# Optimization experiments

Measured on AMD Instinct MI355X. Metric: run time of the kernel, lower is better.

## Reference

```python
import jax, jax.numpy as jnp
import numpy as np

B, N = 8, 8192
S_ATTN, S_NONE = 128, 384          # npoint = (npoint_all=512, npoint_none_attn=384) -> npoint_attn=128
S = S_ATTN + S_NONE
NSAMPLE = 64
RADIUS = 0.4
D_FEAT = 64
MLP = [64, 64, 128]
IN_CH = 3 + D_FEAT


def fps(pts, K):
    # pytorch3d.sample_farthest_points, start index 0, full lengths. pts: [B,N,3]
    B_, N_, _ = pts.shape
    def body(carry, _):
        min_d2, last = carry
        lp = jnp.take_along_axis(pts, last[:, None, None], axis=1)      # [B,1,3]
        d2 = jnp.sum((pts - lp) ** 2, -1)                               # [B,N]
        min_d2 = jnp.minimum(min_d2, d2)
        nxt = jnp.argmax(min_d2, -1).astype(jnp.int32)
        return (min_d2, nxt), last
    init = (jnp.full((B_, N_), jnp.float32(1e10)), jnp.zeros((B_,), jnp.int32))
    _, idxs = jax.lax.scan(body, init, None, length=K)
    idxs = idxs.T                                                       # [B,K]
    sampled = jnp.take_along_axis(pts, idxs[..., None], axis=1)         # [B,K,3]
    return sampled, idxs


def ball_query(query, pts, K, radius):
    # pytorch3d.ball_query: first K points with d2 < r^2 in index order; idx pad=-1, nn pad=0.
    d2 = jnp.sum((query[:, :, None, :] - pts[:, None, :, :]) ** 2, -1)  # [B,S,N]
    mask = d2 < radius * radius
    order = jnp.cumsum(mask.astype(jnp.int32), -1) - 1
    slot = jnp.where(mask & (order < K), order, K)                      # overflow -> dump slot K
    n_ids = jnp.broadcast_to(jnp.arange(pts.shape[1], dtype=jnp.int32), slot.shape)
    def scatter_row(slot_row, ids_row):
        return jnp.full((K + 1,), -1, jnp.int32).at[slot_row].set(ids_row)[:K]
    idx = jax.vmap(jax.vmap(scatter_row))(slot, n_ids)                  # [B,S,K]
    valid = idx >= 0
    gathered = jax.vmap(lambda p, i: p[i])(pts, jnp.where(valid, idx, 0))  # [B,S,K,3]
    nn = jnp.where(valid[..., None], gathered, 0.0)
    return idx, nn


def _forward(xyz, points, attention, ws, bs):
    xyz_t = xyz.transpose(0, 2, 1)            # [B,N,3]
    pts_t = points.transpose(0, 2, 1)         # [B,N,D]
    attn_t = attention.transpose(0, 2, 1)     # [B,N,1]

    attn_xyz = attn_t * xyz_t
    none_xyz = (1.0 - attn_t) * xyz_t
    new_attn_xyz, idx_a = fps(attn_xyz, S_ATTN)
    new_none_xyz, idx_n = fps(none_xyz, S_NONE)
    new_xyz = jnp.concatenate([new_attn_xyz, new_none_xyz], axis=1)     # [B,S,3]
    fps_idx = jnp.concatenate([idx_a, idx_n], axis=1)                   # [B,S]
    new_attention = jnp.take_along_axis(attn_t, fps_idx[..., None], axis=1)  # [B,S,1]

    idx, grouped_xyz = ball_query(new_xyz, xyz_t, NSAMPLE, RADIUS)
    grouped_norm = grouped_xyz - new_xyz[:, :, None, :]                 # [B,S,K,3]
    gather_idx = jnp.where(idx < 0, N - 1, idx)   # torch index -1 wraps to last point
    grouped_pts = jax.vmap(lambda p, i: p[i])(pts_t, gather_idx)        # [B,S,K,D]
    feat = jnp.concatenate([grouped_norm, grouped_pts], -1)             # [B,S,K,3+D]

    x = feat.transpose(0, 3, 2, 1)                                      # [B,C,K,S]
    for w, b in zip(ws, bs):                                            # 1x1 Conv2d + ReLU
        x = jax.nn.relu(jnp.einsum('oc,bcks->boks', w, x) + b[None, :, None, None])
    new_points = jnp.max(x, axis=2)                                     # MaxPool over nsample -> [B,C',S]
    return new_xyz.transpose(0, 2, 1), new_points, new_attention.transpose(0, 2, 1)


def setup_inputs() -> dict:
    key = jax.random.key(0)
    ks = jax.random.split(key, 8)
    xyz = jax.random.normal(ks[0], (B, 3, N), jnp.float32)
    points = jax.random.normal(ks[1], (B, D_FEAT, N), jnp.float32)
    attention = jnp.round(jax.random.uniform(ks[2], (B, 1, N), jnp.float32))  # 0/1 mask
    inp = {'xyz': xyz, 'points': points, 'attention': attention}
    last = IN_CH
    for i, oc in enumerate(MLP):
        inp[f'w{i}'] = jax.random.normal(ks[3 + i], (oc, last), jnp.float32) / np.float32(np.sqrt(last))
        inp[f'b{i}'] = jnp.zeros((oc,), jnp.float32)
        last = oc
    return inp


def reference(xyz, points, attention, w0, b0, w1, b1, w2, b2):
    return _forward(xyz, points, attention, (w0, w1, w2), (b0, b1, b2))
```

## Files before the change

kernel.cpp:

```cpp
#include <hip/hip_runtime.h>
#include <cstdint>
#include <cstddef>

#define NB 8
#define NPTS 8192
#define S_TOT 512
#define NSAMP 64
#define DFEAT 64
#define INCH 67
#define SLOTS 17
#define CCAP (SLOTS * 256)
#define TDONE 1060
#define BALLW 13568

typedef __attribute__((ext_vector_type(8))) short v8s;
typedef __attribute__((ext_vector_type(4))) short v4s;
typedef __attribute__((ext_vector_type(4))) float v4f;

__device__ __forceinline__ float d2_exact(float ax, float ay, float az,
                                          float bx, float by, float bz) {
    float dx = __fsub_rn(ax, bx);
    float dy = __fsub_rn(ay, by);
    float dz = __fsub_rn(az, bz);
    return __fadd_rn(__fadd_rn(__fmul_rn(dx, dx), __fmul_rn(dy, dy)), __fmul_rn(dz, dz));
}

__device__ __forceinline__ unsigned short f2b(float f) {
    unsigned u = __float_as_uint(f);
    return (unsigned short)((u + 0x7fffu + ((u >> 16) & 1u)) >> 16);
}

__device__ __forceinline__ void st_wt_f32(float* p, float v) {
    __hip_atomic_store(p, v, __ATOMIC_RELAXED, __HIP_MEMORY_SCOPE_AGENT);
}
__device__ __forceinline__ void st_wt_u32(unsigned* p, unsigned v) {
    __hip_atomic_store(p, v, __ATOMIC_RELAXED, __HIP_MEMORY_SCOPE_AGENT);
}

template <int CTRL>
__device__ __forceinline__ unsigned long long dpp_max_u64(unsigned long long k) {
    int lo = (int)(unsigned)(k & 0xffffffffull);
    int hi = (int)(unsigned)(k >> 32);
    int slo = __builtin_amdgcn_update_dpp(lo, lo, CTRL, 0xf, 0xf, false);
    int shi = __builtin_amdgcn_update_dpp(hi, hi, CTRL, 0xf, 0xf, false);
    unsigned long long o = ((unsigned long long)(unsigned)shi << 32) | (unsigned)slo;
    return (o > k) ? o : k;
}

__device__ __forceinline__ void ball_one(
    const float* __restrict__ xyz,
    const unsigned short* __restrict__ ptsTh,
    const unsigned short* __restrict__ wp,
    const float* __restrict__ b0, const float* __restrict__ b1,
    const float* __restrict__ b2,
    const float* __restrict__ out0, float* __restrict__ out1,
    int b, int sg, int lane, short* sBuf, int* s_idx)
{
    const float R2 = (float)(0.4 * 0.4);
    int col = lane & 15, quad = lane >> 4, kq = quad * 8;

    const float* xb = xyz + (size_t)b * 3 * NPTS;
    float qx = out0[(size_t)b * 3 * S_TOT + sg];
    float qy = out0[(size_t)b * 3 * S_TOT + S_TOT + sg];
    float qz = out0[(size_t)b * 3 * S_TOT + 2 * S_TOT + sg];

    unsigned long long* s_mask = (unsigned long long*)sBuf;

#pragma unroll 8
    for (int j = 0; j < 128; j++) {
        int n = j * 64 + lane;
        float d2 = d2_exact(qx, qy, qz, xb[n], xb[NPTS + n], xb[2 * NPTS + n]);
        unsigned long long m = __ballot(d2 < R2);
        if (lane == 0) s_mask[j] = m;
    }

    unsigned long long m0 = s_mask[lane];
    unsigned long long m1 = s_mask[64 + lane];
    int c0 = (int)__popcll(m0), c1 = (int)__popcll(m1);
    int i0 = c0;
#pragma unroll
    for (int off = 1; off <= 32; off <<= 1) {
        int t = __shfl_up(i0, off);
        if (lane >= off) i0 += t;
    }
    int T0 = __shfl(i0, 63);
    int i1 = c1;
#pragma unroll
    for (int off = 1; off <= 32; off <<= 1) {
        int t = __shfl_up(i1, off);
        if (lane >= off) i1 += t;
    }
    int total = T0 + __shfl(i1, 63);
    int p0 = i0 - c0;
    int p1 = T0 + i1 - c1;

    {
        int base = p0, org = lane * 64;
        while (m0 && base < NSAMP) {
            int bp = __ffsll((long long)m0) - 1;
            s_idx[base++] = org + bp;
            m0 &= m0 - 1;
        }
        base = p1; org = (64 + lane) * 64;
        while (m1 && base < NSAMP) {
            int bp = __ffsll((long long)m1) - 1;
            s_idx[base++] = org + bp;
            m1 &= m1 - 1;
        }
    }
    int cnt = (total > NSAMP) ? NSAMP : total;

    int nb = (lane < cnt) ? s_idx[lane] : -1;
    float nx_ = 0.f, ny_ = 0.f, nz_ = 0.f;
    if (nb >= 0) { nx_ = xb[nb]; ny_ = xb[NPTS + nb]; nz_ = xb[2 * NPTS + nb]; }
    float fx = nx_ - qx, fy = ny_ - qy, fz = nz_ - qz;
    int row = (nb < 0) ? (NPTS - 1) : nb;

    {
        const unsigned short* ph = ptsTh + ((size_t)b * NPTS + row) * DFEAT;
        short* xr = &sBuf[lane * 104];
#pragma unroll
        for (int i = 0; i < 8; i++)
            *(v8s*)(xr + i * 8) = *(const v8s*)(ph + i * 8);
#pragma unroll
        for (int i = 0; i < 5; i++)
            *(v8s*)(xr + 64 + i * 8) = (v8s)0;
        v4s xyzp;
        xyzp[0] = (short)f2b(fx); xyzp[1] = (short)f2b(fy);
        xyzp[2] = (short)f2b(fz); xyzp[3] = 0;
        *(v4s*)(xr + 64) = xyzp;
    }

    const v8s* wpv = (const v8s*)wp;

    v4f acc[4][4];
#pragma unroll
    for (int nt = 0; nt < 4; nt++) {
        float bb = b0[nt * 16 + col];
#pragma unroll
        for (int mt = 0; mt < 4; mt++) acc[mt][nt] = (v4f){bb, bb, bb, bb};
    }
#pragma unroll
    for (int kt = 0; kt < 3; kt++) {
        v8s bf[4];
#pragma unroll
        for (int nt = 0; nt < 4; nt++) bf[nt] = wpv[(kt * 4 + nt) * 64 + lane];
#pragma unroll
        for (int mt = 0; mt < 4; mt++) {
            v8s a = *(const v8s*)&sBuf[(mt * 16 + col) * 104 + kt * 32 + kq];
#pragma unroll
            for (int nt = 0; nt < 4; nt++)
                acc[mt][nt] = __builtin_amdgcn_mfma_f32_16x16x32_bf16(a, bf[nt], acc[mt][nt], 0, 0, 0);
        }
    }
#pragma unroll
    for (int mt = 0; mt < 4; mt++)
#pragma unroll
        for (int nt = 0; nt < 4; nt++)
#pragma unroll
            for (int r = 0; r < 4; r++)
                sBuf[(mt * 16 + quad * 4 + r) * 72 + nt * 16 + col] =
                    (short)f2b(fmaxf(acc[mt][nt][r], 0.0f));

#pragma unroll
    for (int nt = 0; nt < 4; nt++) {
        float bb = b1[nt * 16 + col];
#pragma unroll
        for (int mt = 0; mt < 4; mt++) acc[mt][nt] = (v4f){bb, bb, bb, bb};
    }
#pragma unroll
    for (int kt = 0; kt < 2; kt++) {
        v8s bf[4];
#pragma unroll
        for (int nt = 0; nt < 4; nt++) bf[nt] = wpv[(12 + kt * 4 + nt) * 64 + lane];
#pragma unroll
        for (int mt = 0; mt < 4; mt++) {
            v8s a = *(const v8s*)&sBuf[(mt * 16 + col) * 72 + kt * 32 + kq];
#pragma unroll
            for (int nt = 0; nt < 4; nt++)
                acc[mt][nt] = __builtin_amdgcn_mfma_f32_16x16x32_bf16(a, bf[nt], acc[mt][nt], 0, 0, 0);
        }
    }
#pragma unroll
    for (int mt = 0; mt < 4; mt++)
#pragma unroll
        for (int nt = 0; nt < 4; nt++)
#pragma unroll
            for (int r = 0; r < 4; r++)
                sBuf[(mt * 16 + quad * 4 + r) * 72 + nt * 16 + col] =
                    (short)f2b(fmaxf(acc[mt][nt][r], 0.0f));

#pragma unroll
    for (int p = 0; p < 2; p++) {
#pragma unroll
        for (int nt = 0; nt < 4; nt++) {
            float bb = b2[(p * 4 + nt) * 16 + col];
#pragma unroll
            for (int mt = 0; mt < 4; mt++) acc[mt][nt] = (v4f){bb, bb, bb, bb};
        }
#pragma unroll
        for (int kt = 0; kt < 2; kt++) {
            v8s bf[4];
#pragma unroll
            for (int nt = 0; nt < 4; nt++)
                bf[nt] = wpv[(20 + kt * 8 + p * 4 + nt) * 64 + lane];
#pragma unroll
            for (int mt = 0; mt < 4; mt++) {
                v8s a = *(const v8s*)&sBuf[(mt * 16 + col) * 72 + kt * 32 + kq];
#pragma unroll
                for (int nt = 0; nt < 4; nt++)
                    acc[mt][nt] = __builtin_amdgcn_mfma_f32_16x16x32_bf16(a, bf[nt], acc[mt][nt], 0, 0, 0);
            }
        }
#pragma unroll
        for (int nt = 0; nt < 4; nt++) {
            float v = 0.0f;
#pragma unroll
            for (int mt = 0; mt < 4; mt++)
#pragma unroll
                for (int r = 0; r < 4; r++)
                    v = fmaxf(v, acc[mt][nt][r]);
            v = fmaxf(v, __shfl_xor(v, 16));
            v = fmaxf(v, __shfl_xor(v, 32));
            if (lane < 16)
                out1[((size_t)(b * 128 + (p * 4 + nt) * 16 + lane)) * S_TOT + sg] = v;
        }
    }
}

__global__ __launch_bounds__(1024) void fps_compact(
    const float* __restrict__ xyz, const float* __restrict__ attn,
    float4* __restrict__ cxyz, int* __restrict__ hdr,
    int* __restrict__ prog, int* __restrict__ tcount, int* __restrict__ skip)
{
    int blk = blockIdx.x;
    int tid = threadIdx.x;
    if (blk == 0) {
        if (tid < 16) prog[tid] = 0;
        if (tid == 16) tcount[0] = 0;
        ((int4*)skip)[tid] = make_int4(0, 0, 0, 0);
    }
    int b = blk >> 1, grp = blk & 1;
    const float* xb = xyz + (size_t)b * 3 * NPTS;
    const float* ab = attn + (size_t)b * NPTS;
    float4* c4 = cxyz + (size_t)blk * CCAP;

    int lane = tid & 63, wid = tid >> 6;
    int n0 = tid * 8;

    __shared__ int s_repmin;
    __shared__ int s_ws[16];
    if (tid == 0) s_repmin = NPTS;
    __syncthreads();

    float av[8];
    *(float4*)&av[0] = *(const float4*)(ab + n0);
    *(float4*)&av[4] = *(const float4*)(ab + n0 + 4);
    int cnt = 0, mymin = NPTS;
    bool keep[8];
#pragma unroll
    for (int j = 0; j < 8; j++) {
        keep[j] = grp ? (av[j] == 0.0f) : (av[j] != 0.0f);
        cnt += keep[j] ? 1 : 0;
        if (!keep[j] && n0 + j < mymin) mymin = n0 + j;
    }
    if (mymin < NPTS) atomicMin(&s_repmin, mymin);

    int incl = cnt;
#pragma unroll
    for (int off = 1; off <= 32; off <<= 1) {
        int t = __shfl_up(incl, off);
        if (lane >= off) incl += t;
    }
    if (lane == 63) s_ws[wid] = incl;
    __syncthreads();
    int woff = 0, tot = 0;
#pragma unroll
    for (int w = 0; w < 16; w++) { if (w < wid) woff += s_ws[w]; tot += s_ws[w]; }
    int pos = woff + incl - cnt;
    int rm = s_repmin;
    int rm_eff = (rm < NPTS) ? rm : 0x7fffffff;

    float xv[8], yv[8], zv[8];
    *(float4*)&xv[0] = *(const float4*)(xb + n0);
    *(float4*)&xv[4] = *(const float4*)(xb + n0 + 4);
    *(float4*)&yv[0] = *(const float4*)(xb + NPTS + n0);
    *(float4*)&yv[4] = *(const float4*)(xb + NPTS + n0 + 4);
    *(float4*)&zv[0] = *(const float4*)(xb + 2 * NPTS + n0);
    *(float4*)&zv[4] = *(const float4*)(xb + 2 * NPTS + n0 + 4);
#pragma unroll
    for (int j = 0; j < 8; j++) {
        if (keep[j]) {
            int fin = pos + ((n0 + j > rm_eff) ? 1 : 0);
            if (fin < CCAP)
                c4[fin] = make_float4(xv[j], yv[j], zv[j], 0.0f);
            pos++;
        }
    }
    if (tid == 0) {
        int M = tot;
        if (rm < NPTS) {
            if (rm < CCAP)
                c4[rm] = make_float4(__fmul_rn(0.0f, xb[rm]),
                                     __fmul_rn(0.0f, xb[NPTS + rm]),
                                     __fmul_rn(0.0f, xb[2 * NPTS + rm]), 0.0f);
            M++;
        }
        hdr[blk * 2] = M;
        hdr[blk * 2 + 1] = (rm < NPTS) ? rm : -1;
    }
}

__global__ __launch_bounds__(256, 1) void fps_fused(
    const float* __restrict__ attn,
    const float4* __restrict__ cxyz,
    const int* __restrict__ hdr,
    float* __restrict__ out0, float* __restrict__ out2,
    const float* __restrict__ pts, unsigned short* __restrict__ ptsTh,
    const float* __restrict__ w0, const float* __restrict__ w1,
    const float* __restrict__ w2, unsigned short* __restrict__ wp,
    const float* __restrict__ xyz,
    const float* __restrict__ b0v, const float* __restrict__ b1v,
    const float* __restrict__ b2v,
    float* __restrict__ out1,
    int* __restrict__ prog, int* __restrict__ tcount, int* __restrict__ skip)
{
    __shared__ __align__(16) char smem[69632 + 6144 + 64];
    int blk = blockIdx.x;
    int tid = threadIdx.x;

    if (blk < 16) {
        int b = blk >> 1, grp = blk & 1;
        int K = grp ? 384 : 128;
        int soff = grp ? 128 : 0;
        int M = hdr[blk * 2];
        int repslot = hdr[blk * 2 + 1];
        if (M > CCAP) {
            if (tid == 0)
                __hip_atomic_store(&prog[blk], -1, __ATOMIC_RELAXED, __HIP_MEMORY_SCOPE_AGENT);
            return;
        }
        int lane = tid & 63, wid = tid >> 6;
        __builtin_amdgcn_s_setprio(1);

        const float4* cb = cxyz + (size_t)blk * CCAP;
        float4* sc = (float4*)smem;
        float4* s_obuf = (float4*)(smem + 69632);
        unsigned long long* s_red = (unsigned long long*)(smem + 69632 + 6144);

        float px[SLOTS], py[SLOTS], pz[SLOTS], md[SLOTS];
#pragma unroll
        for (int i = 0; i < SLOTS; i++) {
            int sl = i * 256 + tid;
            bool v = sl < M;
            float4 c = v ? cb[sl] : make_float4(0.f, 0.f, 0.f, 0.f);
            px[i] = c.x; py[i] = c.y; pz[i] = c.z;
            sc[sl] = c;
            md[i] = v ? 1e10f : -1.0f;
        }
        float4 c0 = cb[0];
        float lx = c0.x, ly = c0.y, lz = c0.z;
        float a_last = attn[(size_t)b * NPTS];
        float kept_a = grp ? 0.0f : 1.0f;
        float rep_a  = grp ? 1.0f : 0.0f;

        for (int k = 0; k < K; k++) {
            if (tid == 0) s_obuf[k] = make_float4(lx, ly, lz, a_last);
            if (k == K - 1) break;

            float bv = -1.0f; int bslot = 0x7fffffff;
#pragma unroll
            for (int i = 0; i < SLOTS; i++) {
                float d2 = d2_exact(px[i], py[i], pz[i], lx, ly, lz);
                md[i] = fminf(md[i], d2);
                int sl = i * 256 + tid;
                bool w = (md[i] > bv) || ((md[i] == bv) && (sl < bslot));
                bv = w ? md[i] : bv;
                bslot = w ? sl : bslot;
            }
            unsigned long long key = (bv >= 0.0f)
                ? (((unsigned long long)__float_as_uint(bv) << 32) | (unsigned)(~bslot))
                : 0ull;
            key = dpp_max_u64<0x111>(key);
            key = dpp_max_u64<0x112>(key);
            key = dpp_max_u64<0x114>(key);
            key = dpp_max_u64<0x118>(key);
            key = dpp_max_u64<0x142>(key);
            key = dpp_max_u64<0x143>(key);
            int buf = k & 1;
            if (lane == 63) s_red[buf * 4 + wid] = key;
            __syncthreads();

            const unsigned long long* rp = &s_red[buf * 4];
            unsigned long long k0 = rp[0], k1 = rp[1], k2 = rp[2], k3 = rp[3];
            unsigned long long m01 = (k0 > k1) ? k0 : k1;
            unsigned long long m23 = (k2 > k3) ? k2 : k3;
            unsigned long long g = (m01 > m23) ? m01 : m23;
            int wslot = (int)(~(unsigned)g);
            float4 wc = sc[wslot];
            lx = wc.x; ly = wc.y; lz = wc.z;
            a_last = (wslot == repslot) ? rep_a : kept_a;

            if (((k & 15) == 15) && wid == 3) {
                if (lane < 16) {
                    int kk = k - 15 + lane;
                    float4 o = s_obuf[kk];
                    int sgO = soff + kk;
                    size_t base = (size_t)b * 3 * S_TOT;
                    st_wt_f32(&out0[base + sgO], o.x);
                    st_wt_f32(&out0[base + S_TOT + sgO], o.y);
                    st_wt_f32(&out0[base + 2 * S_TOT + sgO], o.z);
                    st_wt_f32(&out2[(size_t)b * S_TOT + sgO], o.w);
                }
                asm volatile("s_waitcnt vmcnt(0)" ::: "memory");
                if (lane == 0)
                    __hip_atomic_store(&prog[blk], k + 1, __ATOMIC_RELAXED, __HIP_MEMORY_SCOPE_AGENT);
            }
        }
        __syncthreads();
        if (wid == 3) {
            if (lane < 16) {
                int kk = K - 16 + lane;
                float4 o = s_obuf[kk];
                int sgO = soff + kk;
                size_t base = (size_t)b * 3 * S_TOT;
                st_wt_f32(&out0[base + sgO], o.x);
                st_wt_f32(&out0[base + S_TOT + sgO], o.y);
                st_wt_f32(&out0[base + 2 * S_TOT + sgO], o.z);
                st_wt_f32(&out2[(size_t)b * S_TOT + sgO], o.w);
            }
            asm volatile("s_waitcnt vmcnt(0)" ::: "memory");
            if (lane == 0)
                __hip_atomic_store(&prog[blk], K, __ATOMIC_RELAXED, __HIP_MEMORY_SCOPE_AGENT);
        }
    } else if (blk < 16 + 1024) {
        float (*t)[65] = (float(*)[65])smem;
        int blk2 = blk - 16;
        int b = blk2 >> 7;
        int n0 = (blk2 & 127) * 64;
        int tx = tid & 63, ty = tid >> 6;
        for (int c = ty; c < 64; c += 4)
            t[c][tx] = pts[((size_t)b * DFEAT + c) * NPTS + n0 + tx];
        __syncthreads();
        {
            unsigned* pTu = (unsigned*)ptsTh;
            int txc = tid & 31, rr = tid >> 5;
            for (int r = rr; r < 64; r += 8) {
                unsigned lo = f2b(t[2 * txc][r]);
                unsigned hi = f2b(t[2 * txc + 1][r]);
                st_wt_u32(&pTu[((size_t)b * NPTS + n0 + r) * 32 + txc],
                          lo | (hi << 16));
            }
        }
        asm volatile("s_waitcnt vmcnt(0)" ::: "memory");
        __syncthreads();
        if (tid == 0)
            __hip_atomic_fetch_add(tcount, 1, __ATOMIC_RELAXED, __HIP_MEMORY_SCOPE_AGENT);
    } else if (blk < 1076) {
        if (tid < 64) {
            int t = blk - (16 + 1024), l = tid;
            int kq = (l >> 4) * 8, n16 = l & 15;
            unsigned short o[8];
#pragma unroll
            for (int j = 0; j < 8; j++) {
                float v;
                if (t < 12) {
                    int kt = t >> 2, nt = t & 3;
                    int k = kt * 32 + kq + j, n = nt * 16 + n16;
                    v = (k < 64) ? w0[n * INCH + 3 + k] : (k < 67 ? w0[n * INCH + (k - 64)] : 0.0f);
                } else if (t < 20) {
                    int tt = t - 12, kt = tt >> 2, nt = tt & 3;
                    v = w1[(nt * 16 + n16) * 64 + kt * 32 + kq + j];
                } else {
                    int tt = t - 20, kt = tt >> 3, nt = tt & 7;
                    v = w2[(nt * 16 + n16) * 64 + kt * 32 + kq + j];
                }
                o[j] = f2b(v);
            }
            unsigned* wpu = (unsigned*)wp;
            size_t baseu = (size_t)t * 256 + l * 4;
#pragma unroll
            for (int j = 0; j < 4; j++)
                st_wt_u32(&wpu[baseu + j],
                          (unsigned)o[2 * j] | ((unsigned)o[2 * j + 1] << 16));
            asm volatile("s_waitcnt vmcnt(0)" ::: "memory");
            if (tid == 0)
                __hip_atomic_fetch_add(tcount, 1, __ATOMIC_RELAXED, __HIP_MEMORY_SCOPE_AGENT);
        }
    } else {
        int lane = tid & 63, wid = tid >> 6;
        int w = (blk - 1076) * 4 + wid;
        int b, grp, kk;
        if (w < 2048) { kk = w >> 4; int r = w & 15; b = r & 7; grp = r >> 3; }
        else          { int w2 = w - 2048; kk = 128 + (w2 >> 3); b = w2 & 7; grp = 1; }
        int sg = (grp ? 128 : 0) + kk;
        int q = b * 512 + sg;
        int pblk = b * 2 + grp;

        int ok = 1;
        for (int to = 0;;) {
            int p = __hip_atomic_load(&prog[pblk], __ATOMIC_RELAXED, __HIP_MEMORY_SCOPE_AGENT);
            if (p < 0) { ok = 0; break; }
            if (p > kk) {
                int t = __hip_atomic_load(tcount, __ATOMIC_RELAXED, __HIP_MEMORY_SCOPE_AGENT);
                if (t >= TDONE) break;
            }
            if (++to > 500) { ok = 0; break; }
            __builtin_amdgcn_s_sleep(64);
        }
        if (!ok) {
            if (lane == 0) skip[q] = 1;
            return;
        }
        __builtin_amdgcn_fence(__ATOMIC_ACQUIRE, "agent");

        short* sBufW = (short*)(smem + wid * BALLW);
        int* s_idxW = (int*)(smem + wid * BALLW + 13312);
        ball_one(xyz, ptsTh, wp, b0v, b1v, b2v, out0, out1, b, sg, lane, sBufW, s_idxW);
    }
}

__global__ __launch_bounds__(1024, 1) void fps_kernel(
    const float* __restrict__ xyz, const float* __restrict__ attn,
    const int* __restrict__ hdr,
    float* __restrict__ out0, float* __restrict__ out2)
{
    int blk = blockIdx.x;
    if (hdr != nullptr && hdr[blk * 2] <= CCAP) return;
    int b = blk >> 1, grp = blk & 1;
    int K = grp ? 384 : 128;
    int soff = grp ? 128 : 0;
    int tid = threadIdx.x, lane = tid & 63, wid = tid >> 6;
    const float* xb = xyz + (size_t)b * 3 * NPTS;
    const float* ab = attn + (size_t)b * NPTS;

    float px[8], py[8], pz[8], md[8];
#pragma unroll
    for (int i = 0; i < 8; i++) {
        int n = tid + i * 1024;
        float a = ab[n];
        float f = grp ? __fsub_rn(1.0f, a) : a;
        px[i] = __fmul_rn(f, xb[n]);
        py[i] = __fmul_rn(f, xb[NPTS + n]);
        pz[i] = __fmul_rn(f, xb[2 * NPTS + n]);
        md[i] = 1e10f;
    }
    __shared__ unsigned long long s_red[2][16];
    float a_last = ab[0];
    float f0 = grp ? __fsub_rn(1.0f, a_last) : a_last;
    float lx = __fmul_rn(f0, xb[0]);
    float ly = __fmul_rn(f0, xb[NPTS]);
    float lz = __fmul_rn(f0, xb[2 * NPTS]);

    for (int k = 0; k < K; k++) {
        if (tid == 0) {
            int sg = soff + k;
            out0[(size_t)b * 3 * S_TOT + sg] = lx;
            out0[(size_t)b * 3 * S_TOT + S_TOT + sg] = ly;
            out0[(size_t)b * 3 * S_TOT + 2 * S_TOT + sg] = lz;
            out2[(size_t)b * S_TOT + sg] = a_last;
        }
        if (k == K - 1) break;
        float bv = -1.0f; int bi = 0;
#pragma unroll
        for (int i = 0; i < 8; i++) {
            float d2 = d2_exact(px[i], py[i], pz[i], lx, ly, lz);
            md[i] = fminf(md[i], d2);
            if (md[i] > bv) { bv = md[i]; bi = tid + i * 1024; }
        }
        unsigned long long best =
            ((unsigned long long)__float_as_uint(bv) << 32) | (unsigned)(~bi);
#pragma unroll
        for (int off = 32; off >= 1; off >>= 1) {
            unsigned long long o = __shfl_down(best, off);
            best = (o > best) ? o : best;
        }
        if (lane == 0) s_red[k & 1][wid] = best;
        __syncthreads();
        unsigned long long r = (lane < 16) ? s_red[k & 1][lane] : 0ull;
#pragma unroll
        for (int off = 8; off >= 1; off >>= 1) {
            unsigned long long o = __shfl_down(r, off);
            r = (o > r) ? o : r;
        }
        r = __shfl(r, 0);
        int n = (int)(~(unsigned)r);
        a_last = ab[n];
        float fl = grp ? __fsub_rn(1.0f, a_last) : a_last;
        lx = __fmul_rn(fl, xb[n]);
        ly = __fmul_rn(fl, xb[NPTS + n]);
        lz = __fmul_rn(fl, xb[2 * NPTS + n]);
    }
}

__global__ __launch_bounds__(256) void ball_tail(
    const float* __restrict__ xyz,
    const unsigned short* __restrict__ ptsTh,
    const unsigned short* __restrict__ wp,
    const float* __restrict__ b0, const float* __restrict__ b1,
    const float* __restrict__ b2,
    const float* __restrict__ out0, float* __restrict__ out1,
    const int* __restrict__ skip)
{
    __shared__ __align__(16) char smem[4 * BALLW];
    int lane = threadIdx.x & 63, wid = threadIdx.x >> 6;
    int q = blockIdx.x * 4 + wid;
    if (skip[q] == 0) return;
    int b = q >> 9, sg = q & 511;
    short* sBufW = (short*)(smem + wid * BALLW);
    int* s_idxW = (int*)(smem + wid * BALLW + 13312);
    ball_one(xyz, ptsTh, wp, b0, b1, b2, out0, out1, b, sg, lane, sBufW, s_idxW);
}

__global__ __launch_bounds__(64, 1) void ball_mlp_fb(
    const float* __restrict__ xyz, const float* __restrict__ pts,
    const float* __restrict__ w0, const float* __restrict__ b0,
    const float* __restrict__ w1, const float* __restrict__ b1,
    const float* __restrict__ w2, const float* __restrict__ b2,
    const float* __restrict__ out0, float* __restrict__ out1)
{
    const float R2 = (float)(0.4 * 0.4);
    int q = blockIdx.x;
    int b = q >> 9, sg = q & 511, lane = threadIdx.x;
    const float* xb = xyz + (size_t)b * 3 * NPTS;
    float qx = out0[(size_t)b * 3 * S_TOT + sg];
    float qy = out0[(size_t)b * 3 * S_TOT + S_TOT + sg];
    float qz = out0[(size_t)b * 3 * S_TOT + 2 * S_TOT + sg];

    __shared__ int s_idx[NSAMP];
    __shared__ float s_h[32 * 64];
    int cnt = 0;
    for (int base = 0; base < NPTS; base += 64) {
        int n = base + lane;
        float d2 = d2_exact(qx, qy, qz, xb[n], xb[NPTS + n], xb[2 * NPTS + n]);
        bool flag = d2 < R2;
        unsigned long long m = __ballot(flag);
        int pos = cnt + (int)__popcll(m & ((1ull << lane) - 1ull));
        if (flag && pos < NSAMP) s_idx[pos] = n;
        cnt += (int)__popcll(m);
    }
    if (cnt > NSAMP) cnt = NSAMP;
    int nb = (lane < cnt) ? s_idx[lane] : -1;
    float nx_ = 0.f, ny_ = 0.f, nz_ = 0.f;
    if (nb >= 0) { nx_ = xb[nb]; ny_ = xb[NPTS + nb]; nz_ = xb[2 * NPTS + nb]; }
    float fx = nx_ - qx, fy = ny_ - qy, fz = nz_ - qz;
    int row = (nb < 0) ? (NPTS - 1) : nb;

    float h1[64];
#pragma unroll
    for (int o = 0; o < 64; o++) {
        float a = __builtin_fmaf(w0[o * INCH + 0], fx, b0[o]);
        a = __builtin_fmaf(w0[o * INCH + 1], fy, a);
        h1[o] = __builtin_fmaf(w0[o * INCH + 2], fz, a);
    }
    const float* pb = pts + (size_t)b * DFEAT * NPTS + row;
#pragma unroll 1
    for (int c = 0; c < 64; c++) {
        float f = pb[(size_t)c * NPTS];
#pragma unroll
        for (int o = 0; o < 64; o++)
            h1[o] = __builtin_fmaf(w0[o * INCH + 3 + c], f, h1[o]);
    }
#pragma unroll
    for (int c = 0; c < 32; c++) s_h[c * 64 + lane] = fmaxf(h1[c], 0.0f);
    float h1h[32];
#pragma unroll
    for (int c = 0; c < 32; c++) h1h[c] = fmaxf(h1[32 + c], 0.0f);

    float h2[64];
#pragma unroll
    for (int o = 0; o < 64; o++) h2[o] = b1[o];
#pragma unroll 1
    for (int c = 0; c < 32; c++) {
        float hc = s_h[c * 64 + lane];
#pragma unroll
        for (int o = 0; o < 64; o++)
            h2[o] = __builtin_fmaf(w1[o * 64 + c], hc, h2[o]);
    }
#pragma unroll
    for (int c = 0; c < 32; c++) s_h[c * 64 + lane] = h1h[c];
#pragma unroll 1
    for (int c = 0; c < 32; c++) {
        float hc = s_h[c * 64 + lane];
#pragma unroll
        for (int o = 0; o < 64; o++)
            h2[o] = __builtin_fmaf(w1[o * 64 + (32 + c)], hc, h2[o]);
    }
#pragma unroll
    for (int o = 0; o < 64; o++) h2[o] = fmaxf(h2[o], 0.0f);

#pragma unroll 2
    for (int o = 0; o < 128; o++) {
        const float* wr = w2 + o * 64;
        float acc = b2[o];
#pragma unroll
        for (int c = 0; c < 64; c++) acc = __builtin_fmaf(wr[c], h2[c], acc);
        acc = fmaxf(acc, 0.0f);
#pragma unroll
        for (int off = 32; off >= 1; off >>= 1)
            acc = fmaxf(acc, __shfl_down(acc, off));
        if (lane == 0) out1[((size_t)(b * 128 + o)) * S_TOT + sg] = acc;
    }
}

extern "C" void kernel_launch(void* const* d_in, const int* in_sizes, int n_in,
                              void* d_out, int out_size, void* d_ws, size_t ws_size,
                              hipStream_t stream) {
    const float* xyz  = (const float*)d_in[0];
    const float* pts  = (const float*)d_in[1];
    const float* attn = (const float*)d_in[2];
    const float* w0 = (const float*)d_in[3];
    const float* b0 = (const float*)d_in[4];
    const float* w1 = (const float*)d_in[5];
    const float* b1 = (const float*)d_in[6];
    const float* w2 = (const float*)d_in[7];
    const float* b2 = (const float*)d_in[8];

    float* out0 = (float*)d_out;
    float* out1 = out0 + (size_t)NB * 3 * S_TOT;
    float* out2 = out1 + (size_t)NB * 128 * S_TOT;

    unsigned short* wp    = (unsigned short*)d_ws;
    unsigned short* ptsTh = (unsigned short*)((char*)d_ws + 36864);
    float4*         cxyz  = (float4*)((char*)d_ws + 36864 + 8388608);
    int*            hdr   = (int*)((char*)cxyz + (size_t)16 * CCAP * 16);
    int*            prog  = hdr + 32;
    int*            tcnt  = prog + 16;
    int*            skip  = tcnt + 4;
    const size_t need = 36864 + 8388608 + (size_t)16 * CCAP * 16 + 128
                        + (16 + 4 + 4096) * 4 + 64;

    if (ws_size >= need) {
        fps_compact<<<16, 1024, 0, stream>>>(xyz, attn, cxyz, hdr, prog, tcnt, skip);
        fps_fused<<<16 + 1024 + 36 + 1024, 256, 0, stream>>>(
            attn, cxyz, hdr, out0, out2, pts, ptsTh, w0, w1, w2, wp,
            xyz, b0, b1, b2, out1, prog, tcnt, skip);
        fps_kernel<<<16, 1024, 0, stream>>>(xyz, attn, hdr, out0, out2);
        ball_tail<<<1024, 256, 0, stream>>>(xyz, ptsTh, wp, b0, b1, b2,
                                            out0, out1, skip);
    } else {
        fps_kernel<<<16, 1024, 0, stream>>>(xyz, attn, nullptr, out0, out2);
        ball_mlp_fb<<<NB * S_TOT, 64, 0, stream>>>(xyz, pts, w0, b0, w1, b1,
                                                   w2, b2, out0, out1);
    }
}
```

Measured before the change: 583.8 us.

## Fuse FPS point compaction into persistent FPS blocks and use memset for flags

Removes the separate fps_compact kernel and does the attention-mask compaction inside each FPS block of fps_fused, writing compacted points straight into shared memory and skipping the global cxyz round trip. Progress counters and skip flags are now cleared with hipMemsetAsync instead of inside the kernel. Progress publication is also reordered so each prog update announces the chunk written in the previous batch, which overlaps the output-store wait with later iterations. The serial FPS critical path gains the compaction work, done by 256 threads instead of 1024.

```diff
diff --git a/kernel.cpp b/kernel.cpp
--- a/kernel.cpp
+++ b/kernel.cpp
@@ -228,93 +228,9 @@
     }
 }
 
-__global__ __launch_bounds__(1024) void fps_compact(
-    const float* __restrict__ xyz, const float* __restrict__ attn,
-    float4* __restrict__ cxyz, int* __restrict__ hdr,
-    int* __restrict__ prog, int* __restrict__ tcount, int* __restrict__ skip)
-{
-    int blk = blockIdx.x;
-    int tid = threadIdx.x;
-    if (blk == 0) {
-        if (tid < 16) prog[tid] = 0;
-        if (tid == 16) tcount[0] = 0;
-        ((int4*)skip)[tid] = make_int4(0, 0, 0, 0);
-    }
-    int b = blk >> 1, grp = blk & 1;
-    const float* xb = xyz + (size_t)b * 3 * NPTS;
-    const float* ab = attn + (size_t)b * NPTS;
-    float4* c4 = cxyz + (size_t)blk * CCAP;
-
-    int lane = tid & 63, wid = tid >> 6;
-    int n0 = tid * 8;
-
-    __shared__ int s_repmin;
-    __shared__ int s_ws[16];
-    if (tid == 0) s_repmin = NPTS;
-    __syncthreads();
-
-    float av[8];
-    *(float4*)&av[0] = *(const float4*)(ab + n0);
-    *(float4*)&av[4] = *(const float4*)(ab + n0 + 4);
-    int cnt = 0, mymin = NPTS;
-    bool keep[8];
-#pragma unroll
-    for (int j = 0; j < 8; j++) {
-        keep[j] = grp ? (av[j] == 0.0f) : (av[j] != 0.0f);
-        cnt += keep[j] ? 1 : 0;
-        if (!keep[j] && n0 + j < mymin) mymin = n0 + j;
-    }
-    if (mymin < NPTS) atomicMin(&s_repmin, mymin);
-
-    int incl = cnt;
-#pragma unroll
-    for (int off = 1; off <= 32; off <<= 1) {
-        int t = __shfl_up(incl, off);
-        if (lane >= off) incl += t;
-    }
-    if (lane == 63) s_ws[wid] = incl;
-    __syncthreads();
-    int woff = 0, tot = 0;
-#pragma unroll
-    for (int w = 0; w < 16; w++) { if (w < wid) woff += s_ws[w]; tot += s_ws[w]; }
-    int pos = woff + incl - cnt;
-    int rm = s_repmin;
-    int rm_eff = (rm < NPTS) ? rm : 0x7fffffff;
-
-    float xv[8], yv[8], zv[8];
-    *(float4*)&xv[0] = *(const float4*)(xb + n0);
-    *(float4*)&xv[4] = *(const float4*)(xb + n0 + 4);
-    *(float4*)&yv[0] = *(const float4*)(xb + NPTS + n0);
-    *(float4*)&yv[4] = *(const float4*)(xb + NPTS + n0 + 4);
-    *(float4*)&zv[0] = *(const float4*)(xb + 2 * NPTS + n0);
-    *(float4*)&zv[4] = *(const float4*)(xb + 2 * NPTS + n0 + 4);
-#pragma unroll
-    for (int j = 0; j < 8; j++) {
-        if (keep[j]) {
-            int fin = pos + ((n0 + j > rm_eff) ? 1 : 0);
-            if (fin < CCAP)
-                c4[fin] = make_float4(xv[j], yv[j], zv[j], 0.0f);
-            pos++;
-        }
-    }
-    if (tid == 0) {
-        int M = tot;
-        if (rm < NPTS) {
-            if (rm < CCAP)
-                c4[rm] = make_float4(__fmul_rn(0.0f, xb[rm]),
-                                     __fmul_rn(0.0f, xb[NPTS + rm]),
-                                     __fmul_rn(0.0f, xb[2 * NPTS + rm]), 0.0f);
-            M++;
-        }
-        hdr[blk * 2] = M;
-        hdr[blk * 2 + 1] = (rm < NPTS) ? rm : -1;
-    }
-}
-
 __global__ __launch_bounds__(256, 1) void fps_fused(
     const float* __restrict__ attn,
-    const float4* __restrict__ cxyz,
-    const int* __restrict__ hdr,
+    int* __restrict__ hdr,
     float* __restrict__ out0, float* __restrict__ out2,
     const float* __restrict__ pts, unsigned short* __restrict__ ptsTh,
     const float* __restrict__ w0, const float* __restrict__ w1,
@@ -333,34 +249,101 @@
         int b = blk >> 1, grp = blk & 1;
         int K = grp ? 384 : 128;
         int soff = grp ? 128 : 0;
-        int M = hdr[blk * 2];
-        int repslot = hdr[blk * 2 + 1];
+        int lane = tid & 63, wid = tid >> 6;
+        const float* xb = xyz + (size_t)b * 3 * NPTS;
+        const float* ab = attn + (size_t)b * NPTS;
+
+        float4* sc = (float4*)smem;
+        float4* s_obuf = (float4*)(smem + 69632);
+        unsigned long long* s_red = (unsigned long long*)(smem + 69632 + 6144);
+        int* s_init = (int*)(smem + 69632 + 6144);
+
+        if (tid == 0) s_init[0] = NPTS;
+        __syncthreads();
+
+        int n0 = tid * 32;
+        unsigned km = 0;
+        int cnt = 0;
+#pragma unroll
+        for (int c = 0; c < 8; c++) {
+            float4 a4 = *(const float4*)(ab + n0 + c * 4);
+            const float* af = (const float*)&a4;
+#pragma unroll
+            for (int j = 0; j < 4; j++) {
+                bool kp = grp ? (af[j] == 0.0f) : (af[j] != 0.0f);
+                if (kp) { km |= 1u << (c * 4 + j); cnt++; }
+            }
+        }
+        if (km != 0xFFFFFFFFu)
+            atomicMin(&s_init[0], n0 + __builtin_ctz(~km));
+
+        int incl = cnt;
+#pragma unroll
+        for (int off = 1; off <= 32; off <<= 1) {
+            int t = __shfl_up(incl, off);
+            if (lane >= off) incl += t;
+        }
+        if (lane == 63) s_init[1 + wid] = incl;
+        __syncthreads();
+        int woff = 0, tot = 0;
+#pragma unroll
+        for (int w = 0; w < 4; w++) {
+            int v = s_init[1 + w];
+            if (w < wid) woff += v;
+            tot += v;
+        }
+        int rm = s_init[0];
+        int M = tot + ((rm < NPTS) ? 1 : 0);
+        int repslot = (rm < NPTS) ? rm : -1;
+        if (tid == 0) { hdr[blk * 2] = M; hdr[blk * 2 + 1] = repslot; }
         if (M > CCAP) {
             if (tid == 0)
                 __hip_atomic_store(&prog[blk], -1, __ATOMIC_RELAXED, __HIP_MEMORY_SCOPE_AGENT);
             return;
         }
-        int lane = tid & 63, wid = tid >> 6;
+        int pos = woff + incl - cnt;
+        int rm_eff = (rm < NPTS) ? rm : 0x7fffffff;
+#pragma unroll
+        for (int c = 0; c < 8; c++) {
+            if ((km >> (c * 4)) & 0xFu) {
+                float4 xx = *(const float4*)(xb + n0 + c * 4);
+                float4 yy = *(const float4*)(xb + NPTS + n0 + c * 4);
+                float4 zz = *(const float4*)(xb + 2 * NPTS + n0 + c * 4);
+                const float* xf = (const float*)&xx;
+                const float* yf = (const float*)&yy;
+                const float* zf = (const float*)&zz;
+#pragma unroll
+                for (int j = 0; j < 4; j++) {
+                    if ((km >> (c * 4 + j)) & 1u) {
+                        int idx = n0 + c * 4 + j;
+                        int fin = pos + ((idx > rm_eff) ? 1 : 0);
+                        sc[fin] = make_float4(xf[j], yf[j], zf[j], 0.0f);
+                        pos++;
+                    }
+                }
+            }
+        }
+        if (tid == 0 && rm < NPTS)
+            sc[rm] = make_float4(__fmul_rn(0.0f, xb[rm]),
+                                 __fmul_rn(0.0f, xb[NPTS + rm]),
+                                 __fmul_rn(0.0f, xb[2 * NPTS + rm]), 0.0f);
+        __syncthreads();
         __builtin_amdgcn_s_setprio(1);
-
-        const float4* cb = cxyz + (size_t)blk * CCAP;
-        float4* sc = (float4*)smem;
-        float4* s_obuf = (float4*)(smem + 69632);
-        unsigned long long* s_red = (unsigned long long*)(smem + 69632 + 6144);
 
         float px[SLOTS], py[SLOTS], pz[SLOTS], md[SLOTS];
 #pragma unroll
         for (int i = 0; i < SLOTS; i++) {
             int sl = i * 256 + tid;
             bool v = sl < M;
-            float4 c = v ? cb[sl] : make_float4(0.f, 0.f, 0.f, 0.f);
-            px[i] = c.x; py[i] = c.y; pz[i] = c.z;
-            sc[sl] = c;
+            float4 c = sc[sl];
+            px[i] = v ? c.x : 0.0f;
+            py[i] = v ? c.y : 0.0f;
+            pz[i] = v ? c.z : 0.0f;
             md[i] = v ? 1e10f : -1.0f;
         }
-        float4 c0 = cb[0];
+        float4 c0 = sc[0];
         float lx = c0.x, ly = c0.y, lz = c0.z;
-        float a_last = attn[(size_t)b * NPTS];
+        float a_last = ab[0];
         float kept_a = grp ? 0.0f : 1.0f;
         float rep_a  = grp ? 1.0f : 0.0f;
 
@@ -402,6 +385,9 @@
             a_last = (wslot == repslot) ? rep_a : kept_a;
 
             if (((k & 15) == 15) && wid == 3) {
+                asm volatile("s_waitcnt vmcnt(0)" ::: "memory");
+                if (lane == 0 && k >= 31)
+                    __hip_atomic_store(&prog[blk], k - 15, __ATOMIC_RELAXED, __HIP_MEMORY_SCOPE_AGENT);
                 if (lane < 16) {
                     int kk = k - 15 + lane;
                     float4 o = s_obuf[kk];
@@ -412,9 +398,6 @@
                     st_wt_f32(&out0[base + 2 * S_TOT + sgO], o.z);
                     st_wt_f32(&out2[(size_t)b * S_TOT + sgO], o.w);
                 }
-                asm volatile("s_waitcnt vmcnt(0)" ::: "memory");
-                if (lane == 0)
-                    __hip_atomic_store(&prog[blk], k + 1, __ATOMIC_RELAXED, __HIP_MEMORY_SCOPE_AGENT);
             }
         }
         __syncthreads();
@@ -722,8 +705,8 @@
 
     unsigned short* wp    = (unsigned short*)d_ws;
     unsigned short* ptsTh = (unsigned short*)((char*)d_ws + 36864);
-    float4*         cxyz  = (float4*)((char*)d_ws + 36864 + 8388608);
-    int*            hdr   = (int*)((char*)cxyz + (size_t)16 * CCAP * 16);
+    char*           cxyz  = (char*)d_ws + 36864 + 8388608;
+    int*            hdr   = (int*)(cxyz + (size_t)16 * CCAP * 16);
     int*            prog  = hdr + 32;
     int*            tcnt  = prog + 16;
     int*            skip  = tcnt + 4;
@@ -731,9 +714,9 @@
                         + (16 + 4 + 4096) * 4 + 64;
 
     if (ws_size >= need) {
-        fps_compact<<<16, 1024, 0, stream>>>(xyz, attn, cxyz, hdr, prog, tcnt, skip);
+        hipMemsetAsync(prog, 0, (size_t)(16 + 4 + 4096) * 4, stream);
         fps_fused<<<16 + 1024 + 36 + 1024, 256, 0, stream>>>(
-            attn, cxyz, hdr, out0, out2, pts, ptsTh, w0, w1, w2, wp,
+            attn, hdr, out0, out2, pts, ptsTh, w0, w1, w2, wp,
             xyz, b0, b1, b2, out1, prog, tcnt, skip);
         fps_kernel<<<16, 1024, 0, stream>>>(xyz, attn, hdr, out0, out2);
         ball_tail<<<1024, 256, 0, stream>>>(xyz, ptsTh, wp, b0, b1, b2,
```

After: 611.5 us. 1.05x slower.
